# Kernel optimization log

Measured on AMD Instinct MI355X. Metric: run time of the kernel, lower is better.

## Reference

```python
import jax, jax.numpy as jnp
import numpy as np

EPS = 1e-08


def setup_inputs() -> dict:
    key = jax.random.key(0)
    X = jax.random.normal(key, (16384, 768), dtype=jnp.float32)
    return {"X": X}


def reference(X) -> jnp.ndarray:
    # L2-normalize rows (torch F.normalize with eps: divide by max(norm, eps))
    norms = jnp.linalg.norm(X, axis=-1, keepdims=True)
    Xn = X / jnp.maximum(norms, EPS)

    n = Xn.shape[0]
    # pairwise inner products [n, n]; mask self-similarity on diagonal with -1
    dots = Xn @ Xn.T
    dots = jnp.where(jnp.eye(n, dtype=bool), jnp.float32(-1.0), dots)
    I = jnp.argmax(dots, axis=1)  # nearest neighbor index per row

    # torch PairwiseDistance(2, eps): ||x - y + eps||_2
    diff = Xn - Xn[I] + EPS
    distances = jnp.linalg.norm(diff, axis=-1)

    # loss_type == 'standard'
    loss = -jnp.mean(jnp.log(distances + EPS))
    return loss
```

## Files before the change

kernel.cpp:

```cpp
#include <hip/hip_runtime.h>
#include <hip/hip_bf16.h>
#include <stdint.h>
#include <math.h>

#define NR 16384
#define DIM 768
#define KEPS 1e-8f

#define BM 128
#define BK 64
#define NB (NR / BM)
#define KT (DIM / BK)
#define NTILES (NB * (NB + 1) / 2)

typedef __attribute__((ext_vector_type(4))) float f32x4;

__device__ inline uint32_t fkey(float f) {
    union { float f; uint32_t u; } v; v.f = f;
    return (v.u & 0x80000000u) ? ~v.u : (v.u | 0x80000000u);
}

__device__ inline unsigned long long pack_vc(float v, int c) {
    return ((unsigned long long)fkey(v) << 32) | (unsigned)c;
}

__device__ inline void gload16(const uint8_t* g, const uint8_t* l) {
    __builtin_amdgcn_global_load_lds(
        (const __attribute__((address_space(1))) void*)g,
        (__attribute__((address_space(3))) void*)l,
        16, 0, 0);
}

__device__ inline uint8_t f2fp8(float f) {
    union { float f; uint32_t u; } v; v.f = f;
    const uint8_t s = (uint8_t)((v.u >> 24) & 0x80u);
    float a = fabsf(f);
    if (a >= 448.0f) return s | 0x7E;
    if (a < 0.015625f) {
        int q = (int)rintf(a * 512.0f);
        if (q >= 8) return s | 0x08;
        return s | (uint8_t)q;
    }
    int ex; float m = frexpf(a, &ex);
    int E = ex + 6;
    int frac = (int)rintf(m * 16.0f - 8.0f);
    if (frac >= 8) { frac = 0; ++E; if (E > 15) return s | 0x7E; }
    return s | (uint8_t)(E << 3) | (uint8_t)frac;
}

__global__ __launch_bounds__(256) void k_norm(const float* __restrict__ X,
                                              uint8_t* __restrict__ Xn,
                                              float* __restrict__ norms) {
    __shared__ uint8_t buf[4][768];
    const int wid = threadIdx.x >> 6, lane = threadIdx.x & 63;
    const int row = blockIdx.x * 4 + wid;
    const float4* xr = (const float4*)(X + (size_t)row * DIM) + lane * 3;
    float4 a = xr[0], b = xr[1], c = xr[2];
    float s = a.x*a.x + a.y*a.y + a.z*a.z + a.w*a.w
            + b.x*b.x + b.y*b.y + b.z*b.z + b.w*b.w
            + c.x*c.x + c.y*c.y + c.z*c.z + c.w*c.w;
#pragma unroll
    for (int m = 32; m >= 1; m >>= 1) s += __shfl_xor(s, m);
    const float n = sqrtf(s);
    if (lane == 0) norms[row] = n;
    const float rn = 1.0f / fmaxf(n, KEPS);
    float v[12] = {a.x,a.y,a.z,a.w,b.x,b.y,b.z,b.w,c.x,c.y,c.z,c.w};
    uint8_t q[12];
#pragma unroll
    for (int i = 0; i < 12; ++i) q[i] = f2fp8(v[i] * rn);
    uint32_t* lb = (uint32_t*)&buf[wid][lane * 12];
    lb[0] = (uint32_t)q[0] | ((uint32_t)q[1] << 8) | ((uint32_t)q[2]  << 16) | ((uint32_t)q[3]  << 24);
    lb[1] = (uint32_t)q[4] | ((uint32_t)q[5] << 8) | ((uint32_t)q[6]  << 16) | ((uint32_t)q[7]  << 24);
    lb[2] = (uint32_t)q[8] | ((uint32_t)q[9] << 8) | ((uint32_t)q[10] << 16) | ((uint32_t)q[11] << 24);
    __syncthreads();
    if (lane < 48) {
        const uint2* pb = (const uint2*)&buf[wid][lane * 16];
        uint2 lo = pb[0], hi = pb[1];
        uint4 o;
        if (row & 8) o = make_uint4(hi.x, hi.y, lo.x, lo.y);
        else         o = make_uint4(lo.x, lo.y, hi.x, hi.y);
        *(uint4*)(Xn + (size_t)row * DIM + lane * 16) = o;
    }
}

__global__ __launch_bounds__(256) void k_init(unsigned long long* __restrict__ nn64) {
    nn64[blockIdx.x * 256 + threadIdx.x] = pack_vc(-2.0f, 0);
}

__global__ __launch_bounds__(256, 4) void k_maxdot(const uint8_t* __restrict__ Xn,
                                                   unsigned long long* __restrict__ nn64) {
    __shared__ uint8_t lA[BM * BK];
    __shared__ uint8_t lB[BM * BK];
    const int tid  = threadIdx.x;
    const int lane = tid & 63, wid = tid >> 6;
    const int wr = wid >> 1, wc = wid & 1;
    const int l15 = lane & 15, lhi = lane >> 4;

    int t = (int)blockIdx.x;
    t = (t & 7) * (NTILES / 8) + (t >> 3);
    float disc = 66049.0f - 8.0f * (float)t;
    int rb = (int)((257.0f - sqrtf(disc)) * 0.5f);
    if (rb > NB - 1) rb = NB - 1;
    if (rb < 0) rb = 0;
    while (rb > 0 && rb * (257 - rb) / 2 > t) --rb;
    while ((rb + 1) * (257 - (rb + 1)) / 2 <= t) ++rb;
    const int cb = rb + (t - rb * (257 - rb) / 2);
    const int rowbase = rb * BM;
    const int colbase = cb * BM;
    const bool diag = (rb == cb);

    f32x4 acc[4][4];
    const f32x4 z = {0.f, 0.f, 0.f, 0.f};
#pragma unroll
    for (int i = 0; i < 4; ++i)
#pragma unroll
        for (int j = 0; j < 4; ++j) acc[i][j] = z;

    const int s_r0 = tid >> 2;
    const int s_c  = tid & 3;

    for (int kt = 0; kt < KT; ++kt) {
#pragma unroll
        for (int it = 0; it < 2; ++it) {
            const int r = it * 64 + s_r0;
            const int c = s_c ^ ((r >> 1) & 3);
            const size_t koff = (size_t)kt * BK + c * 16;
            gload16(Xn + (size_t)(rowbase + r) * DIM + koff, lA + it * 4096 + wid * 1024);
            gload16(Xn + (size_t)(colbase + r) * DIM + koff, lB + it * 4096 + wid * 1024);
        }
        __syncthreads();
#pragma unroll
        for (int ks = 0; ks < 2; ++ks) {
            long af[4], bg[4];
            const int s16 = ks * 2 + (lhi >> 1);
            const int lo8 = (lhi & 1) * 8;
#pragma unroll
            for (int mf = 0; mf < 4; ++mf) {
                const int r = wr * 64 + mf * 16 + l15;
                af[mf] = *(const long*)(lA + r * 64 + ((s16 ^ ((r >> 1) & 3)) << 4) + (lo8 ^ (r & 8)));
            }
#pragma unroll
            for (int nf = 0; nf < 4; ++nf) {
                const int r = wc * 64 + nf * 16 + l15;
                bg[nf] = *(const long*)(lB + r * 64 + ((s16 ^ ((r >> 1) & 3)) << 4) + (lo8 ^ (r & 8)));
            }
#pragma unroll
            for (int mf = 0; mf < 4; ++mf)
#pragma unroll
                for (int nf = 0; nf < 4; ++nf)
                    acc[mf][nf] = __builtin_amdgcn_mfma_f32_16x16x32_fp8_fp8(
                        af[mf], bg[nf], acc[mf][nf], 0, 0, 0);
        }
        __syncthreads();
    }

    if (diag) {
#pragma unroll
        for (int mf = 0; mf < 4; ++mf)
#pragma unroll
            for (int nf = 0; nf < 4; ++nf)
#pragma unroll
                for (int rr = 0; rr < 4; ++rr) {
                    const int rl = wr * 64 + mf * 16 + lhi * 4 + rr;
                    const int cl = wc * 64 + nf * 16 + l15;
                    if (rl == cl) acc[mf][nf][rr] = -1.0f;
                }
    }

#pragma unroll
    for (int mf = 0; mf < 4; ++mf)
#pragma unroll
        for (int rr = 0; rr < 4; ++rr) {
            float v = acc[mf][0][rr];
            int   c = colbase + wc * 64 + l15;
#pragma unroll
            for (int nf = 1; nf < 4; ++nf) {
                const float w2 = acc[mf][nf][rr];
                const int   c2 = colbase + wc * 64 + nf * 16 + l15;
                if (w2 > v) { v = w2; c = c2; }
            }
#pragma unroll
            for (int m = 1; m <= 8; m <<= 1) {
                const float ov = __shfl_xor(v, m);
                const int   oc = __shfl_xor(c, m);
                if (ov > v) { v = ov; c = oc; }
            }
            if (l15 == 0) {
                const int r = rowbase + wr * 64 + mf * 16 + lhi * 4 + rr;
                atomicMax(&nn64[r], pack_vc(v, c));
            }
        }

#pragma unroll
    for (int nf = 0; nf < 4; ++nf) {
        float v = acc[0][nf][0];
        int   c = rowbase + wr * 64 + lhi * 4;
#pragma unroll
        for (int mf = 0; mf < 4; ++mf)
#pragma unroll
            for (int rr = 0; rr < 4; ++rr) {
                if (mf == 0 && rr == 0) continue;
                const float w2 = acc[mf][nf][rr];
                const int   c2 = rowbase + wr * 64 + mf * 16 + lhi * 4 + rr;
                if (w2 > v) { v = w2; c = c2; }
            }
#pragma unroll
        for (int m = 16; m <= 32; m <<= 1) {
            const float ov = __shfl_xor(v, m);
            const int   oc = __shfl_xor(c, m);
            if (ov > v) { v = ov; c = oc; }
        }
        if ((lane >> 4) == 0) {
            const int cc = colbase + wc * 64 + nf * 16 + l15;
            atomicMax(&nn64[cc], pack_vc(v, c));
        }
    }
}

__global__ __launch_bounds__(256) void k_refine(const float* __restrict__ X,
                                                const float* __restrict__ norms,
                                                const unsigned long long* __restrict__ nn64,
                                                float* __restrict__ logd) {
    const int wid = threadIdx.x >> 6, lane = threadIdx.x & 63;
    const int r = blockIdx.x * 4 + wid;
    const int j = (int)(nn64[r] & 0xFFFFu);
    const float rnr = 1.0f / fmaxf(norms[r], KEPS);
    const float rnj = 1.0f / fmaxf(norms[j], KEPS);
    const float4* xr = (const float4*)(X + (size_t)r * DIM) + lane * 3;
    const float4* xj = (const float4*)(X + (size_t)j * DIM) + lane * 3;
    float s = 0.0f;
#pragma unroll
    for (int i = 0; i < 3; ++i) {
        const float4 a = xr[i], b = xj[i];
        float d;
        d = a.x * rnr - b.x * rnj + KEPS; s = fmaf(d, d, s);
        d = a.y * rnr - b.y * rnj + KEPS; s = fmaf(d, d, s);
        d = a.z * rnr - b.z * rnj + KEPS; s = fmaf(d, d, s);
        d = a.w * rnr - b.w * rnj + KEPS; s = fmaf(d, d, s);
    }
#pragma unroll
    for (int m = 32; m >= 1; m >>= 1) s += __shfl_xor(s, m);
    if (lane == 0) logd[r] = logf(sqrtf(s) + KEPS);
}

__global__ __launch_bounds__(256) void k_loss(const float* __restrict__ logd,
                                              float* __restrict__ out) {
    float local = 0.0f;
    for (int r = threadIdx.x; r < NR; r += 256) local += logd[r];
#pragma unroll
    for (int m = 32; m >= 1; m >>= 1) local += __shfl_xor(local, m);
    __shared__ float red[4];
    const int lane = threadIdx.x & 63, wid = threadIdx.x >> 6;
    if (lane == 0) red[wid] = local;
    __syncthreads();
    if (threadIdx.x == 0)
        out[0] = -(red[0] + red[1] + red[2] + red[3]) / (float)NR;
}

extern "C" void kernel_launch(void* const* d_in, const int* in_sizes, int n_in,
                              void* d_out, int out_size, void* d_ws, size_t ws_size,
                              hipStream_t stream) {
    const float* X = (const float*)d_in[0];
    float* out = (float*)d_out;
    uint8_t* Xn = (uint8_t*)d_ws;
    char* p = (char*)d_ws + (size_t)NR * DIM;
    float* norms = (float*)p;                 p += (size_t)NR * 4;
    unsigned long long* nn64 = (unsigned long long*)p; p += (size_t)NR * 8;
    float* logd = (float*)p;

    k_norm<<<NR / 4, 256, 0, stream>>>(X, Xn, norms);
    k_init<<<NR / 256, 256, 0, stream>>>(nn64);
    k_maxdot<<<NTILES, 256, 0, stream>>>(Xn, nn64);
    k_refine<<<NR / 4, 256, 0, stream>>>(X, norms, nn64, logd);
    k_loss<<<1, 256, 0, stream>>>(logd, out);
}
```

Measured before the change: 307.9 us.

## Use 16x16x128 scaled FP8 MFMA with BK=128 and new LDS swizzle

Switches the fp8 dot-product GEMM from the 16x16x32 MFMA to the MI355's scaled 16x16x128 f8f6f4 MFMA with unit scales, doubling the K tile to 128 so each k-step issues one instruction per fragment. The LDS layout swizzle is changed to an XOR over 8 16-byte chunks, and the normalization kernel now writes rows unpermuted to match. Launch bounds occupancy hint drops from 4 to 3 to accommodate doubled LDS and larger fragment registers. The aim is higher MFMA throughput and fewer instructions, at the cost of lower occupancy.

```diff
diff --git a/kernel.cpp b/kernel.cpp
--- a/kernel.cpp
+++ b/kernel.cpp
@@ -8,12 +8,13 @@
 #define KEPS 1e-8f
 
 #define BM 128
-#define BK 64
+#define BK 128
 #define NB (NR / BM)
 #define KT (DIM / BK)
 #define NTILES (NB * (NB + 1) / 2)
 
 typedef __attribute__((ext_vector_type(4))) float f32x4;
+typedef __attribute__((ext_vector_type(8))) int   i32x8;
 
 __device__ inline uint32_t fkey(float f) {
     union { float f; uint32_t u; } v; v.f = f;
@@ -73,21 +74,15 @@
     lb[1] = (uint32_t)q[4] | ((uint32_t)q[5] << 8) | ((uint32_t)q[6]  << 16) | ((uint32_t)q[7]  << 24);
     lb[2] = (uint32_t)q[8] | ((uint32_t)q[9] << 8) | ((uint32_t)q[10] << 16) | ((uint32_t)q[11] << 24);
     __syncthreads();
-    if (lane < 48) {
-        const uint2* pb = (const uint2*)&buf[wid][lane * 16];
-        uint2 lo = pb[0], hi = pb[1];
-        uint4 o;
-        if (row & 8) o = make_uint4(hi.x, hi.y, lo.x, lo.y);
-        else         o = make_uint4(lo.x, lo.y, hi.x, hi.y);
-        *(uint4*)(Xn + (size_t)row * DIM + lane * 16) = o;
-    }
+    if (lane < 48)
+        *(uint4*)(Xn + (size_t)row * DIM + lane * 16) = *(const uint4*)&buf[wid][lane * 16];
 }
 
 __global__ __launch_bounds__(256) void k_init(unsigned long long* __restrict__ nn64) {
     nn64[blockIdx.x * 256 + threadIdx.x] = pack_vc(-2.0f, 0);
 }
 
-__global__ __launch_bounds__(256, 4) void k_maxdot(const uint8_t* __restrict__ Xn,
+__global__ __launch_bounds__(256, 3) void k_maxdot(const uint8_t* __restrict__ Xn,
                                                    unsigned long long* __restrict__ nn64) {
     __shared__ uint8_t lA[BM * BK];
     __shared__ uint8_t lB[BM * BK];
@@ -116,41 +111,44 @@
 #pragma unroll
         for (int j = 0; j < 4; ++j) acc[i][j] = z;
 
-    const int s_r0 = tid >> 2;
-    const int s_c  = tid & 3;
+    const int s_r0 = tid >> 3;
+    const int s_c  = tid & 7;
+
+    auto RDF = [&](const uint8_t* base, int r) -> i32x8 {
+        const int rs = r & 7;
+        const uint8_t* p = base + r * BK;
+        const int4 lo = *(const int4*)(p + ((((lhi << 1))     ^ rs) << 4));
+        const int4 hi = *(const int4*)(p + ((((lhi << 1) | 1) ^ rs) << 4));
+        i32x8 v;
+        v[0] = lo.x; v[1] = lo.y; v[2] = lo.z; v[3] = lo.w;
+        v[4] = hi.x; v[5] = hi.y; v[6] = hi.z; v[7] = hi.w;
+        return v;
+    };
 
     for (int kt = 0; kt < KT; ++kt) {
 #pragma unroll
-        for (int it = 0; it < 2; ++it) {
-            const int r = it * 64 + s_r0;
-            const int c = s_c ^ ((r >> 1) & 3);
+        for (int it = 0; it < 4; ++it) {
+            const int r = it * 32 + s_r0;
+            const int c = s_c ^ (r & 7);
             const size_t koff = (size_t)kt * BK + c * 16;
-            gload16(Xn + (size_t)(rowbase + r) * DIM + koff, lA + it * 4096 + wid * 1024);
-            gload16(Xn + (size_t)(colbase + r) * DIM + koff, lB + it * 4096 + wid * 1024);
+            gload16(Xn + (size_t)(rowbase + r) * DIM + koff, lA + it * 4096 + tid * 16);
+            gload16(Xn + (size_t)(colbase + r) * DIM + koff, lB + it * 4096 + tid * 16);
         }
         __syncthreads();
-#pragma unroll
-        for (int ks = 0; ks < 2; ++ks) {
-            long af[4], bg[4];
-            const int s16 = ks * 2 + (lhi >> 1);
-            const int lo8 = (lhi & 1) * 8;
-#pragma unroll
-            for (int mf = 0; mf < 4; ++mf) {
-                const int r = wr * 64 + mf * 16 + l15;
-                af[mf] = *(const long*)(lA + r * 64 + ((s16 ^ ((r >> 1) & 3)) << 4) + (lo8 ^ (r & 8)));
-            }
-#pragma unroll
-            for (int nf = 0; nf < 4; ++nf) {
-                const int r = wc * 64 + nf * 16 + l15;
-                bg[nf] = *(const long*)(lB + r * 64 + ((s16 ^ ((r >> 1) & 3)) << 4) + (lo8 ^ (r & 8)));
-            }
-#pragma unroll
-            for (int mf = 0; mf < 4; ++mf)
-#pragma unroll
-                for (int nf = 0; nf < 4; ++nf)
-                    acc[mf][nf] = __builtin_amdgcn_mfma_f32_16x16x32_fp8_fp8(
-                        af[mf], bg[nf], acc[mf][nf], 0, 0, 0);
-        }
+        i32x8 af[4], bg[4];
+#pragma unroll
+        for (int mf = 0; mf < 4; ++mf) af[mf] = RDF(lA, wr * 64 + mf * 16 + l15);
+#pragma unroll
+        for (int nf = 0; nf < 4; ++nf) bg[nf] = RDF(lB, wc * 64 + nf * 16 + l15);
+#pragma unroll
+        for (int mf = 0; mf < 4; ++mf)
+#pragma unroll
+            for (int nf = 0; nf < 4; ++nf)
+                acc[mf][nf] = __builtin_amdgcn_mfma_scale_f32_16x16x128_f8f6f4(
+                    af[mf], bg[nf], acc[mf][nf],
+                    0, 0,
+                    0, 0x7F,
+                    0, 0x7F);
         __syncthreads();
     }
 
```

After: 1.116 ms. +262.5%, slower.
